# Kernel tuning notes

Hardware: AMD Instinct MI355X
Metric: run time of the kernel (lower is better)

Reference implementation:

```python
import jax, jax.numpy as jnp
import numpy as np

B, C_IN, HW = 4096, 3, 32
NUM_MODULES, NUM_AGENTS, OUT_DIM = 16, 10, 10
FEAT = 128
HID = 48
BN_EPS = 1e-5


def _conv_block(x, w, b):
    # x: [B,C,H,W], w: [O,I,3,3] -> conv(pad=1) + ReLU + maxpool2
    y = jax.lax.conv_general_dilated(
        x, w, window_strides=(1, 1), padding=((1, 1), (1, 1)),
        dimension_numbers=("NCHW", "OIHW", "NCHW"))
    y = jax.nn.relu(y + b[None, :, None, None])
    return jax.lax.reduce_window(y, -jnp.inf, jax.lax.max,
                                 (1, 1, 2, 2), (1, 1, 2, 2), "VALID")


def setup_inputs() -> dict:
    key = jax.random.key(0)
    ks = jax.random.split(key, 24)

    def lin(k, shape, fan_in):
        return (jax.random.normal(k, shape, dtype=jnp.float32) / np.sqrt(fan_in)).astype(jnp.float32)

    inp = {
        "x": jax.random.normal(ks[0], (B, C_IN, HW, HW), dtype=jnp.float32),
        "tasks": jax.random.randint(ks[1], (B,), 0, NUM_AGENTS, dtype=jnp.int32),
        # conv backbone
        "cw1": lin(ks[2], (32, C_IN, 3, 3), C_IN * 9), "cb1": jnp.zeros((32,), jnp.float32),
        "cw2": lin(ks[3], (32, 32, 3, 3), 32 * 9),     "cb2": jnp.zeros((32,), jnp.float32),
        "cw3": lin(ks[4], (32, 32, 3, 3), 32 * 9),     "cb3": jnp.zeros((32,), jnp.float32),
        "cw4": lin(ks[5], (32, 32, 3, 3), 32 * 9),     "cb4": jnp.zeros((32,), jnp.float32),
        "bn_g": jnp.ones((32,), jnp.float32), "bn_b": jnp.zeros((32,), jnp.float32),
        # routing policies (approx linear policies)
        "wpt": lin(ks[6], (FEAT, NUM_AGENTS), FEAT),                  # per-task assignment (1 agent)
        "wd1": lin(ks[7], (NUM_AGENTS, FEAT, NUM_MODULES), FEAT),    # per-agent decision 1
        "wd2": lin(ks[8], (NUM_AGENTS, HID, NUM_MODULES), HID),      # per-agent decision 2
        "wd3": lin(ks[9], (NUM_AGENTS, HID, NUM_MODULES), HID),      # per-agent decision 3
        # expert banks (stacked Linear layers, stored [in,out])
        "s1_w": lin(ks[10], (NUM_MODULES, FEAT, HID), FEAT), "s1_b": jnp.zeros((NUM_MODULES, HID), jnp.float32),
        "s2_w": lin(ks[11], (NUM_MODULES, HID, HID), HID),   "s2_b": jnp.zeros((NUM_MODULES, HID), jnp.float32),
        "s3_w": lin(ks[12], (NUM_MODULES, HID, OUT_DIM), HID), "s3_b": jnp.zeros((NUM_MODULES, OUT_DIM), jnp.float32),
    }
    return inp


def _decide(feat, wd, agents):
    # gather per-sample agent policy, pick argmax action
    logits = jnp.einsum("bf,bfm->bm", feat, wd[agents])  # [B, num_modules]
    return jnp.argmax(logits, axis=-1)


def _select(feat, w_bank, b_bank, actions, relu=True):
    # per-sample expert gather -> small GEMM -> scatter back (vectorized)
    y = jnp.einsum("bf,bfo->bo", feat, w_bank[actions]) + b_bank[actions]
    return jax.nn.relu(y) if relu else y


def reference(x, tasks, cw1, cb1, cw2, cb2, cw3, cb3, cw4, cb4, bn_g, bn_b,
              wpt, wd1, wd2, wd3, s1_w, s1_b, s2_w, s2_b, s3_w, s3_b):
    y = _conv_block(x, cw1, cb1)
    y = _conv_block(y, cw2, cb2)
    y = _conv_block(y, cw3, cb3)
    y = _conv_block(y, cw4, cb4)
    # BatchNorm2d (training-mode batch stats)
    mu = jnp.mean(y, axis=(0, 2, 3), keepdims=True)
    var = jnp.var(y, axis=(0, 2, 3), keepdims=True)
    y = (y - mu) * jax.lax.rsqrt(var + BN_EPS) * bn_g[None, :, None, None] + bn_b[None, :, None, None]
    y = y.reshape(y.shape[0], -1)  # [B, 128]

    # per-task assignment: single-agent policy picks the agent id per sample
    task_actions = jnp.argmax(y @ wpt, axis=-1)  # [B]

    a1 = _decide(y, wd1, task_actions)
    y = _select(y, s1_w, s1_b, a1, relu=True)
    a2 = _decide(y, wd2, task_actions)
    y = _select(y, s2_w, s2_b, a2, relu=True)
    a3 = _decide(y, wd3, task_actions)
    y = _select(y, s3_w, s3_b, a3, relu=False)
    return y
```

## Files before the change

kernel.cpp:

```cpp
#include <hip/hip_runtime.h>
#include <math.h>


#define IMG_B 4096

typedef _Float16 f16x8 __attribute__((ext_vector_type(8)));
typedef _Float16 f16x4 __attribute__((ext_vector_type(4)));
typedef float    f32x4 __attribute__((ext_vector_type(4)));

union U16x8 { unsigned u[4]; f16x8 v; };

__device__ inline f16x8 f16x8_zero() {
    f16x8 z;
    #pragma unroll
    for (int i = 0; i < 8; ++i) z[i] = (_Float16)0.f;
    return z;
}

__global__ __launch_bounds__(256) void twt_kernel(
    const float* __restrict__ cw1, const float* __restrict__ cw2,
    const float* __restrict__ cw3, const float* __restrict__ cw4,
    _Float16* __restrict__ w1s, _Float16* __restrict__ w2s,
    _Float16* __restrict__ w3s, _Float16* __restrict__ w4s)
{
    const int i = blockIdx.x * 256 + threadIdx.x;
    if (i < 2048) {
        const int p = i >> 10, rr = i & 1023;
        const int oc = rr >> 5, k = rr & 31;
        _Float16 val = (_Float16)0.f;
        if (k < 27) {
            float w = cw1[oc * 27 + k];
            _Float16 h = (_Float16)w;
            val = p ? (_Float16)(w - (float)h) : h;
        }
        w1s[p * 1024 + oc * 32 + k] = val;
    }
    if (i < 9216) {
        const int k = i % 9, r = i / 9;
        const int ic2 = r & 31, oc2 = r >> 5;
        {
            float w = cw2[(oc2 * 32 + ic2) * 9 + k];
            _Float16 h = (_Float16)w;
            w2s[(k * 2 + 0) * 1024 + oc2 * 32 + ic2] = h;
            w2s[(k * 2 + 1) * 1024 + oc2 * 32 + ic2] = (_Float16)(w - (float)h);
        }
        {
            float w = cw3[(oc2 * 32 + ic2) * 9 + k];
            _Float16 h = (_Float16)w;
            w3s[(k * 2 + 0) * 1024 + oc2 * 32 + ic2] = h;
            w3s[(k * 2 + 1) * 1024 + oc2 * 32 + ic2] = (_Float16)(w - (float)h);
        }
        {
            float w = cw4[(oc2 * 32 + ic2) * 9 + k];
            _Float16 h = (_Float16)w;
            w4s[(k * 2 + 0) * 1024 + oc2 * 32 + ic2] = h;
            w4s[(k * 2 + 1) * 1024 + oc2 * 32 + ic2] = (_Float16)(w - (float)h);
        }
    }
}

__global__ __launch_bounds__(512, 6) void backbone_kernel(
    const float* __restrict__ x,
    const _Float16* __restrict__ w1s, const float* __restrict__ cb1,
    const _Float16* __restrict__ w2s, const float* __restrict__ cb2,
    const _Float16* __restrict__ w3s, const float* __restrict__ cb3,
    const _Float16* __restrict__ w4s, const float* __restrict__ cb4,
    float* __restrict__ t4)
{
    __shared__ __align__(16) unsigned char smem[50736];
    _Float16* b1h = (_Float16*)smem;
    _Float16* b1l = (_Float16*)(smem + 18432);
    unsigned char* region2 = smem + 36864;
    unsigned* sxu = (unsigned*)region2;
    _Float16* b2h = (_Float16*)region2;
    _Float16* b2l = (_Float16*)(region2 + 4096);
    _Float16* b3h = (_Float16*)(region2 + 8192);
    _Float16* b3l = (_Float16*)(region2 + 10496);
    float*    scr = (float*)region2;

    const int t = threadIdx.x;
    const int b = blockIdx.x;
    const int lane = t & 63;
    const int w  = __builtin_amdgcn_readfirstlane(t >> 6);
    const int wr = w >> 1;
    const int mh = w & 1;
    const int xl = lane & 15;
    const int g  = lane >> 4;
    const int aoff = xl * 32 + g * 8;

    for (int i = t; i < 3468; i += 512) sxu[i] = 0;
    for (int i = t; i < 1024; i += 512) {
        const int j = i & 15, cs = (i >> 4) & 1, r = (i >> 5) & 15, P = i >> 9;
        ((unsigned*)(smem + P * 18432))[(r * 18 + (cs ? 17 : 0)) * 16 + j] = 0;
    }
    __syncthreads();

    {
        const float* xb = x + (size_t)b * 3072;
        for (int i = t; i < 3072; i += 512) {
            const int ic = i >> 10, r = i & 1023;
            const float v = xb[i];
            const _Float16 h = (_Float16)v;
            const _Float16 l = (_Float16)(v - (float)h);
            const unsigned hu = (unsigned)__builtin_bit_cast(unsigned short, h);
            const unsigned lu = (unsigned)__builtin_bit_cast(unsigned short, l);
            sxu[ic * 1156 + ((r >> 5) + 1) * 34 + (r & 31) + 1] = hu | (lu << 16);
        }
    }
    __syncthreads();

    {
        const f16x8 ah0 = *(const f16x8*)(w1s + xl * 32 + g * 8);
        const f16x8 ah1 = *(const f16x8*)(w1s + (16 + xl) * 32 + g * 8);
        const f16x8 al0 = *(const f16x8*)(w1s + 1024 + xl * 32 + g * 8);
        const f16x8 al1 = *(const f16x8*)(w1s + 1024 + (16 + xl) * 32 + g * 8);
        const f32x4 cbias0 = *(const f32x4*)(cb1 + g * 4);
        const f32x4 cbias1 = *(const f32x4*)(cb1 + 16 + g * 4);

        int off_j[8];
        #pragma unroll
        for (int j = 0; j < 8; ++j) {
            int k = g * 8 + j; if (k > 26) k = 26;
            const int ic = k / 9, t9 = k - ic * 9;
            const int dy = t9 / 3, dx = t9 - dy * 3;
            off_j[j] = ic * 1156 + dy * 34 + dx;
        }

        for (int q = 0; q < 2; ++q) {
            const int rp = w * 2 + q;
            const int y0 = 2 * rp;
            for (int xt = 0; xt < 2; ++xt) {
                const int xpix = xt * 16 + xl;
                f32x4 acc[2][2];
                #pragma unroll
                for (int yy = 0; yy < 2; ++yy)
                    #pragma unroll
                    for (int m = 0; m < 2; ++m)
                        #pragma unroll
                        for (int r = 0; r < 4; ++r) acc[yy][m][r] = 0.f;
                #pragma unroll
                for (int yy = 0; yy < 2; ++yy) {
                    const int base = (y0 + yy) * 34 + xpix;
                    unsigned e[8];
                    #pragma unroll
                    for (int j = 0; j < 8; ++j) e[j] = sxu[off_j[j] + base];
                    U16x8 Bh, Bl;
                    #pragma unroll
                    for (int p = 0; p < 4; ++p) {
                        const unsigned e0 = e[2 * p], e1 = e[2 * p + 1];
                        Bh.u[p] = (e0 & 0xffffu) | (e1 << 16);
                        Bl.u[p] = (e0 >> 16) | (e1 & 0xffff0000u);
                    }
                    acc[yy][0] = __builtin_amdgcn_mfma_f32_16x16x32_f16(ah0, Bh.v, acc[yy][0], 0, 0, 0);
                    acc[yy][0] = __builtin_amdgcn_mfma_f32_16x16x32_f16(ah0, Bl.v, acc[yy][0], 0, 0, 0);
                    acc[yy][0] = __builtin_amdgcn_mfma_f32_16x16x32_f16(al0, Bh.v, acc[yy][0], 0, 0, 0);
                    acc[yy][1] = __builtin_amdgcn_mfma_f32_16x16x32_f16(ah1, Bh.v, acc[yy][1], 0, 0, 0);
                    acc[yy][1] = __builtin_amdgcn_mfma_f32_16x16x32_f16(ah1, Bl.v, acc[yy][1], 0, 0, 0);
                    acc[yy][1] = __builtin_amdgcn_mfma_f32_16x16x32_f16(al1, Bh.v, acc[yy][1], 0, 0, 0);
                }
                #pragma unroll
                for (int m = 0; m < 2; ++m) {
                    f32x4 vv;
                    #pragma unroll
                    for (int r = 0; r < 4; ++r) {
                        float v = fmaxf(acc[0][m][r], acc[1][m][r]);
                        v = fmaxf(v, __shfl_xor(v, 1));
                        vv[r] = fmaxf(v + (m ? cbias1[r] : cbias0[r]), 0.f);
                    }
                    if ((xl & 1) == 0) {
                        const int c = xt * 8 + (xl >> 1) + 1;
                        const int grp = m * 2 + (g >> 1);
                        const int so = (grp + (c >> 1)) & 3;
                        const int e = (rp * 18 + c) * 32 + so * 8 + (g & 1) * 4;
                        f16x4 h4, l4;
                        #pragma unroll
                        for (int r = 0; r < 4; ++r) {
                            const _Float16 h = (_Float16)vv[r];
                            h4[r] = h;
                            l4[r] = (_Float16)(vv[r] - (float)h);
                        }
                        *(f16x4*)(b1h + e) = h4;
                        *(f16x4*)(b1l + e) = l4;
                    }
                }
            }
        }
    }
    __syncthreads();

    {
        for (int i = t; i < 1152; i += 512) ((unsigned*)(region2 + 8192))[i] = 0;

        f32x4 acc[2][2];
        #pragma unroll
        for (int j = 0; j < 2; ++j)
            #pragma unroll
            for (int m = 0; m < 2; ++m)
                #pragma unroll
                for (int r = 0; r < 4; ++r) acc[j][m][r] = 0.f;

        #pragma unroll
        for (int dy = 0; dy < 3; ++dy) {
            #pragma unroll
            for (int dx = 0; dx < 3; ++dx) {
                const _Float16* wb = w2s + (dy * 3 + dx) * 2048;
                const f16x8 ah0 = *(const f16x8*)(wb + aoff);
                const f16x8 ah1 = *(const f16x8*)(wb + 512 + aoff);
                const f16x8 al0 = *(const f16x8*)(wb + 1024 + aoff);
                const f16x8 al1 = *(const f16x8*)(wb + 1536 + aoff);

                const int cxs = xl + dx;
                const int so = (g + (cxs >> 1)) & 3;
                #pragma unroll
                for (int j = 0; j < 2; ++j) {
                    const int sy = 2 * w + j + dy - 1;
                    if ((unsigned)sy < 16u) {
                        const int e = (sy * 18 + cxs) * 32 + so * 8;
                        const f16x8 bh = *(const f16x8*)(b1h + e);
                        const f16x8 bl = *(const f16x8*)(b1l + e);
                        acc[j][0] = __builtin_amdgcn_mfma_f32_16x16x32_f16(ah0, bh, acc[j][0], 0, 0, 0);
                        acc[j][0] = __builtin_amdgcn_mfma_f32_16x16x32_f16(ah0, bl, acc[j][0], 0, 0, 0);
                        acc[j][0] = __builtin_amdgcn_mfma_f32_16x16x32_f16(al0, bh, acc[j][0], 0, 0, 0);
                        acc[j][1] = __builtin_amdgcn_mfma_f32_16x16x32_f16(ah1, bh, acc[j][1], 0, 0, 0);
                        acc[j][1] = __builtin_amdgcn_mfma_f32_16x16x32_f16(ah1, bl, acc[j][1], 0, 0, 0);
                        acc[j][1] = __builtin_amdgcn_mfma_f32_16x16x32_f16(al1, bh, acc[j][1], 0, 0, 0);
                    }
                }
            }
        }

        const f32x4 bias0 = *(const f32x4*)(cb2 + g * 4);
        const f32x4 bias1 = *(const f32x4*)(cb2 + 16 + g * 4);
        #pragma unroll
        for (int m = 0; m < 2; ++m) {
            f32x4 vv;
            #pragma unroll
            for (int r = 0; r < 4; ++r) {
                float v = fmaxf(acc[0][m][r], acc[1][m][r]);
                v = fmaxf(v, __shfl_xor(v, 1));
                vv[r] = fmaxf(v + (m ? bias1[r] : bias0[r]), 0.f);
            }
            if ((lane & 1) == 0) {
                const int pp = w * 8 + (xl >> 1);
                const int slot = m * 2 + (g >> 1);
                const int so2 = (slot + (pp >> 1)) & 3;
                const int e = pp * 32 + so2 * 8 + (g & 1) * 4;
                f16x4 h4, l4;
                #pragma unroll
                for (int r = 0; r < 4; ++r) {
                    const _Float16 h = (_Float16)vv[r];
                    h4[r] = h;
                    l4[r] = (_Float16)(vv[r] - (float)h);
                }
                *(f16x4*)(b2h + e) = h4;
                *(f16x4*)(b2l + e) = l4;
            }
        }
    }
    __syncthreads();

    {
        const int p = wr * 16 + xl;
        const int py3 = p >> 3, px3 = p & 7;
        f32x4 acc;
        #pragma unroll
        for (int r = 0; r < 4; ++r) acc[r] = 0.f;

        #pragma unroll
        for (int dy = 0; dy < 3; ++dy) {
            #pragma unroll
            for (int dx = 0; dx < 3; ++dx) {
                const _Float16* wb = w3s + (dy * 3 + dx) * 2048 + mh * 512;
                const f16x8 ah = *(const f16x8*)(wb + aoff);
                const f16x8 al = *(const f16x8*)(wb + 1024 + aoff);

                const int syL = py3 + dy - 1, sxL = px3 + dx - 1;
                const bool ok = ((unsigned)syL < 8u) && ((unsigned)sxL < 8u);
                const int cy = syL < 0 ? 0 : (syL > 7 ? 7 : syL);
                const int cx = sxL < 0 ? 0 : (sxL > 7 ? 7 : sxL);
                const int cp = cy * 8 + cx;
                const int so = (g + (cp >> 1)) & 3;
                const int e = cp * 32 + so * 8;
                f16x8 bh = *(const f16x8*)(b2h + e);
                f16x8 bl = *(const f16x8*)(b2l + e);
                if (!ok) { bh = f16x8_zero(); bl = f16x8_zero(); }
                acc = __builtin_amdgcn_mfma_f32_16x16x32_f16(ah, bh, acc, 0, 0, 0);
                acc = __builtin_amdgcn_mfma_f32_16x16x32_f16(ah, bl, acc, 0, 0, 0);
                acc = __builtin_amdgcn_mfma_f32_16x16x32_f16(al, bh, acc, 0, 0, 0);
            }
        }

        const f32x4 bias = *(const f32x4*)(cb3 + mh * 16 + g * 4);
        f32x4 vv;
        #pragma unroll
        for (int r = 0; r < 4; ++r) {
            float v = acc[r];
            v = fmaxf(v, __shfl_xor(v, 1));
            v = fmaxf(v, __shfl_xor(v, 8));
            vv[r] = fmaxf(v + bias[r], 0.f);
        }
        if ((lane & 9) == 0) {
            const int yr = wr;
            const int xr = (xl & 7) >> 1;
            const int pp3 = (yr + 1) * 6 + (xr + 1);
            const int grp = mh * 2 + (g >> 1);
            const int so = (grp + (pp3 >> 1)) & 3;
            const int e = pp3 * 32 + so * 8 + (g & 1) * 4;
            f16x4 h4, l4;
            #pragma unroll
            for (int r = 0; r < 4; ++r) {
                const _Float16 h = (_Float16)vv[r];
                h4[r] = h;
                l4[r] = (_Float16)(vv[r] - (float)h);
            }
            *(f16x4*)(b3h + e) = h4;
            *(f16x4*)(b3l + e) = l4;
        }
    }
    __syncthreads();

    {
        f32x4 a4;
        #pragma unroll
        for (int r = 0; r < 4; ++r) a4[r] = 0.f;

        for (int t9 = wr; t9 < 9; t9 += 4) {
            const _Float16* wb = w4s + t9 * 2048 + mh * 512;
            const f16x8 ah = *(const f16x8*)(wb + aoff);
            const f16x8 al = *(const f16x8*)(wb + 1024 + aoff);
            const int dy = t9 / 3, dx = t9 - dy * 3;
            const int pp3 = ((xl >> 2) + dy) * 6 + (xl & 3) + dx;
            const int so = (g + (pp3 >> 1)) & 3;
            const int e = pp3 * 32 + so * 8;
            const f16x8 bh = *(const f16x8*)(b3h + e);
            const f16x8 bl = *(const f16x8*)(b3l + e);
            a4 = __builtin_amdgcn_mfma_f32_16x16x32_f16(ah, bh, a4, 0, 0, 0);
            a4 = __builtin_amdgcn_mfma_f32_16x16x32_f16(ah, bl, a4, 0, 0, 0);
            a4 = __builtin_amdgcn_mfma_f32_16x16x32_f16(al, bh, a4, 0, 0, 0);
        }
        *(f32x4*)(scr + (w * 64 + lane) * 4) = a4;
        __syncthreads();

        if (w < 2) {
            f32x4 r0;
            #pragma unroll
            for (int r = 0; r < 4; ++r) r0[r] = 0.f;
            #pragma unroll
            for (int k = 0; k < 4; ++k) {
                const f32x4 p0 = *(const f32x4*)(scr + ((k * 2 + w) * 64 + lane) * 4);
                #pragma unroll
                for (int r = 0; r < 4; ++r) r0[r] += p0[r];
            }
            const f32x4 bias = *(const f32x4*)(cb4 + w * 16 + g * 4);
            const int y = xl >> 2, xx = xl & 3;
            f32x4 vv;
            #pragma unroll
            for (int r = 0; r < 4; ++r) {
                float v = r0[r];
                v = fmaxf(v, __shfl_xor(v, 1));
                v = fmaxf(v, __shfl_xor(v, 4));
                vv[r] = fmaxf(v + bias[r], 0.f);
            }
            if ((xl & 5) == 0) {
                const int oc0 = w * 16 + g * 4;
                #pragma unroll
                for (int r = 0; r < 4; ++r)
                    t4[(size_t)b * 128 + (oc0 + r) * 4 + (y >> 1) * 2 + (xx >> 1)] = vv[r];
            }
        }
    }
}

__global__ __launch_bounds__(256) void bnstats_kernel(
    const float* __restrict__ t4, float* __restrict__ mus, float* __restrict__ rss)
{
    __shared__ double ssum[256];
    __shared__ double ssq[256];
    const int c = blockIdx.x, t = threadIdx.x;
    double s = 0.0, q = 0.0;
    for (int j = t; j < 16384; j += 256) {
        float v = t4[(size_t)(j >> 2) * 128 + c * 4 + (j & 3)];
        s += (double)v;
        q += (double)v * (double)v;
    }
    ssum[t] = s; ssq[t] = q;
    __syncthreads();
    for (int w = 128; w > 0; w >>= 1) {
        if (t < w) { ssum[t] += ssum[t + w]; ssq[t] += ssq[t + w]; }
        __syncthreads();
    }
    if (t == 0) {
        double mu = ssum[0] / 16384.0;
        double var = ssq[0] / 16384.0 - mu * mu;
        mus[c] = (float)mu;
        rss[c] = (float)(1.0 / sqrt(var + 1e-5));
    }
}

__global__ __launch_bounds__(64) void routing_kernel(
    const float* __restrict__ t4, const float* __restrict__ mus,
    const float* __restrict__ rss,
    const float* __restrict__ bng, const float* __restrict__ bnb,
    const float* __restrict__ wpt, const float* __restrict__ wd1,
    const float* __restrict__ wd2, const float* __restrict__ wd3,
    const float* __restrict__ s1w, const float* __restrict__ s1b,
    const float* __restrict__ s2w, const float* __restrict__ s2b,
    const float* __restrict__ s3w, const float* __restrict__ s3b,
    float* __restrict__ out)
{
    __shared__ float f[128];
    __shared__ float h1s[48];
    __shared__ float h2s[48];
    __shared__ float tmp[16];
    __shared__ int act;
    const int t = threadIdx.x, b = blockIdx.x;

    for (int i = t; i < 128; i += 64) {
        int c = i >> 2;
        float v = t4[(size_t)b * 128 + i];
        f[i] = (v - mus[c]) * rss[c] * bng[c] + bnb[c];
    }
    __syncthreads();

    if (t < 10) {
        double a = 0.0;
        for (int k = 0; k < 128; ++k) a = fma((double)f[k], (double)wpt[k * 10 + t], a);
        tmp[t] = (float)a;
    }
    __syncthreads();
    if (t == 0) {
        int bi = 0; float bv = tmp[0];
        for (int i = 1; i < 10; ++i) if (tmp[i] > bv) { bv = tmp[i]; bi = i; }
        act = bi;
    }
    __syncthreads();
    const int agent = act;

    if (t < 16) {
        double a = 0.0;
        const float* wd = wd1 + (size_t)agent * 128 * 16 + t;
        for (int k = 0; k < 128; ++k) a = fma((double)f[k], (double)wd[k * 16], a);
        tmp[t] = (float)a;
    }
    __syncthreads();
    if (t == 0) {
        int bi = 0; float bv = tmp[0];
        for (int i = 1; i < 16; ++i) if (tmp[i] > bv) { bv = tmp[i]; bi = i; }
        act = bi;
    }
    __syncthreads();
    const int a1 = act;

    if (t < 48) {
        float a = s1b[a1 * 48 + t];
        const float* wd = s1w + (size_t)a1 * 128 * 48 + t;
        for (int k = 0; k < 128; ++k) a = fmaf(f[k], wd[k * 48], a);
        h1s[t] = fmaxf(a, 0.f);
    }
    __syncthreads();

    if (t < 16) {
        double a = 0.0;
        const float* wd = wd2 + (size_t)agent * 48 * 16 + t;
        for (int k = 0; k < 48; ++k) a = fma((double)h1s[k], (double)wd[k * 16], a);
        tmp[t] = (float)a;
    }
    __syncthreads();
    if (t == 0) {
        int bi = 0; float bv = tmp[0];
        for (int i = 1; i < 16; ++i) if (tmp[i] > bv) { bv = tmp[i]; bi = i; }
        act = bi;
    }
    __syncthreads();
    const int a2 = act;

    if (t < 48) {
        float a = s2b[a2 * 48 + t];
        const float* wd = s2w + (size_t)a2 * 48 * 48 + t;
        for (int k = 0; k < 48; ++k) a = fmaf(h1s[k], wd[k * 48], a);
        h2s[t] = fmaxf(a, 0.f);
    }
    __syncthreads();

    if (t < 16) {
        double a = 0.0;
        const float* wd = wd3 + (size_t)agent * 48 * 16 + t;
        for (int k = 0; k < 48; ++k) a = fma((double)h2s[k], (double)wd[k * 16], a);
        tmp[t] = (float)a;
    }
    __syncthreads();
    if (t == 0) {
        int bi = 0; float bv = tmp[0];
        for (int i = 1; i < 16; ++i) if (tmp[i] > bv) { bv = tmp[i]; bi = i; }
        act = bi;
    }
    __syncthreads();
    const int a3 = act;

    if (t < 10) {
        float a = s3b[a3 * 10 + t];
        const float* wd = s3w + (size_t)a3 * 48 * 10 + t;
        for (int k = 0; k < 48; ++k) a = fmaf(h2s[k], wd[k * 10], a);
        out[(size_t)b * 10 + t] = a;
    }
}

extern "C" void kernel_launch(void* const* d_in, const int* in_sizes, int n_in,
                              void* d_out, int out_size, void* d_ws, size_t ws_size,
                              hipStream_t stream)
{
    (void)in_sizes; (void)n_in; (void)out_size; (void)ws_size;

    const float* x   = (const float*)d_in[0];
    const float* cw1 = (const float*)d_in[2];
    const float* cb1 = (const float*)d_in[3];
    const float* cw2 = (const float*)d_in[4];
    const float* cb2 = (const float*)d_in[5];
    const float* cw3 = (const float*)d_in[6];
    const float* cb3 = (const float*)d_in[7];
    const float* cw4 = (const float*)d_in[8];
    const float* cb4 = (const float*)d_in[9];
    const float* bng = (const float*)d_in[10];
    const float* bnb = (const float*)d_in[11];
    const float* wpt = (const float*)d_in[12];
    const float* wd1 = (const float*)d_in[13];
    const float* wd2 = (const float*)d_in[14];
    const float* wd3 = (const float*)d_in[15];
    const float* s1w = (const float*)d_in[16];
    const float* s1b = (const float*)d_in[17];
    const float* s2w = (const float*)d_in[18];
    const float* s2b = (const float*)d_in[19];
    const float* s3w = (const float*)d_in[20];
    const float* s3b = (const float*)d_in[21];
    float* out = (float*)d_out;

    float* t4  = (float*)d_ws;
    float* mus = t4 + (size_t)IMG_B * 128;
    float* rss = mus + 32;
    _Float16* w1s = (_Float16*)(rss + 32);
    _Float16* w2s = w1s + 2048;
    _Float16* w3s = w2s + 18432;
    _Float16* w4s = w3s + 18432;

    hipLaunchKernelGGL(twt_kernel, dim3(36), dim3(256), 0, stream,
                       cw1, cw2, cw3, cw4, w1s, w2s, w3s, w4s);
    hipLaunchKernelGGL(backbone_kernel, dim3(IMG_B), dim3(512), 0, stream,
                       x, w1s, cb1, w2s, cb2, w3s, cb3, w4s, cb4, t4);
    hipLaunchKernelGGL(bnstats_kernel, dim3(32), dim3(256), 0, stream, t4, mus, rss);
    hipLaunchKernelGGL(routing_kernel, dim3(IMG_B), dim3(64), 0, stream,
                       t4, mus, rss, bng, bnb, wpt, wd1, wd2, wd3,
                       s1w, s1b, s2w, s2b, s3w, s3b, out);
}
```

Measured before the change: 194.7 us.

## Zero only input halo, use byte-perm packing, and wave-level routing argmax

The backbone kernel now zeros only the halo border of the padded input tile instead of the whole buffer, and drops one block barrier before loading the input. The hi/lo f16 packing uses v_perm instead of shift/mask sequences. The routing kernel packs four samples per 256-thread block, one wave each, and replaces the shared-memory serial argmax and block barriers with shuffle-based wave argmax and wave barriers. Removing the barrier relies on halo zeroing and interior writes touching disjoint addresses. Ties in the argmax now resolve to the lowest index, as before, and the comparison is done in double rather than float.

```diff
diff --git a/kernel.cpp b/kernel.cpp
--- a/kernel.cpp
+++ b/kernel.cpp
@@ -88,13 +88,19 @@
     const int g  = lane >> 4;
     const int aoff = xl * 32 + g * 8;
 
-    for (int i = t; i < 3468; i += 512) sxu[i] = 0;
+    for (int i = t; i < 396; i += 512) {
+        const int p = i / 132, r = i - p * 132;
+        int row, col;
+        if (r < 34)       { row = 0;       col = r; }
+        else if (r < 68)  { row = 33;      col = r - 34; }
+        else if (r < 100) { row = r - 67;  col = 0; }
+        else              { row = r - 99;  col = 33; }
+        sxu[p * 1156 + row * 34 + col] = 0;
+    }
     for (int i = t; i < 1024; i += 512) {
         const int j = i & 15, cs = (i >> 4) & 1, r = (i >> 5) & 15, P = i >> 9;
         ((unsigned*)(smem + P * 18432))[(r * 18 + (cs ? 17 : 0)) * 16 + j] = 0;
     }
-    __syncthreads();
-
     {
         const float* xb = x + (size_t)b * 3072;
         for (int i = t; i < 3072; i += 512) {
@@ -104,7 +110,8 @@
             const _Float16 l = (_Float16)(v - (float)h);
             const unsigned hu = (unsigned)__builtin_bit_cast(unsigned short, h);
             const unsigned lu = (unsigned)__builtin_bit_cast(unsigned short, l);
-            sxu[ic * 1156 + ((r >> 5) + 1) * 34 + (r & 31) + 1] = hu | (lu << 16);
+            sxu[ic * 1156 + ((r >> 5) + 1) * 34 + (r & 31) + 1] =
+                __builtin_amdgcn_perm(lu, hu, 0x05040100u);
         }
     }
     __syncthreads();
@@ -148,8 +155,8 @@
                     #pragma unroll
                     for (int p = 0; p < 4; ++p) {
                         const unsigned e0 = e[2 * p], e1 = e[2 * p + 1];
-                        Bh.u[p] = (e0 & 0xffffu) | (e1 << 16);
-                        Bl.u[p] = (e0 >> 16) | (e1 & 0xffff0000u);
+                        Bh.u[p] = __builtin_amdgcn_perm(e1, e0, 0x05040100u);
+                        Bl.u[p] = __builtin_amdgcn_perm(e1, e0, 0x07060302u);
                     }
                     acc[yy][0] = __builtin_amdgcn_mfma_f32_16x16x32_f16(ah0, Bh.v, acc[yy][0], 0, 0, 0);
                     acc[yy][0] = __builtin_amdgcn_mfma_f32_16x16x32_f16(ah0, Bl.v, acc[yy][0], 0, 0, 0);
@@ -397,7 +404,17 @@
     }
 }
 
-__global__ __launch_bounds__(64) void routing_kernel(
+__device__ __forceinline__ int wave_argmax16(double v, int idx) {
+    #pragma unroll
+    for (int d = 8; d >= 1; d >>= 1) {
+        const double ov = __shfl_xor(v, d);
+        const int oi = __shfl_xor(idx, d);
+        if (ov > v || (ov == v && oi < idx)) { v = ov; idx = oi; }
+    }
+    return __shfl(idx, 0);
+}
+
+__global__ __launch_bounds__(256) void routing_kernel(
     const float* __restrict__ t4, const float* __restrict__ mus,
     const float* __restrict__ rss,
     const float* __restrict__ bng, const float* __restrict__ bnb,
@@ -408,100 +425,75 @@
     const float* __restrict__ s3w, const float* __restrict__ s3b,
     float* __restrict__ out)
 {
-    __shared__ float f[128];
-    __shared__ float h1s[48];
-    __shared__ float h2s[48];
-    __shared__ float tmp[16];
-    __shared__ int act;
-    const int t = threadIdx.x, b = blockIdx.x;
+    __shared__ float fs[4][128];
+    __shared__ float h1s[4][48];
+    __shared__ float h2s[4][48];
+    const int t = threadIdx.x & 63;
+    const int w = threadIdx.x >> 6;
+    const int b = blockIdx.x * 4 + w;
+    float* fw  = fs[w];
+    float* h1w = h1s[w];
+    float* h2w = h2s[w];
 
     for (int i = t; i < 128; i += 64) {
-        int c = i >> 2;
-        float v = t4[(size_t)b * 128 + i];
-        f[i] = (v - mus[c]) * rss[c] * bng[c] + bnb[c];
-    }
-    __syncthreads();
-
+        const int c = i >> 2;
+        const float v = t4[(size_t)b * 128 + i];
+        fw[i] = (v - mus[c]) * rss[c] * bng[c] + bnb[c];
+    }
+    __builtin_amdgcn_wave_barrier();
+
+    double a = -INFINITY;
     if (t < 10) {
-        double a = 0.0;
-        for (int k = 0; k < 128; ++k) a = fma((double)f[k], (double)wpt[k * 10 + t], a);
-        tmp[t] = (float)a;
-    }
-    __syncthreads();
-    if (t == 0) {
-        int bi = 0; float bv = tmp[0];
-        for (int i = 1; i < 10; ++i) if (tmp[i] > bv) { bv = tmp[i]; bi = i; }
-        act = bi;
-    }
-    __syncthreads();
-    const int agent = act;
-
+        a = 0.0;
+        for (int k = 0; k < 128; ++k) a = fma((double)fw[k], (double)wpt[k * 10 + t], a);
+    }
+    const int agent = wave_argmax16(a, t & 15);
+
+    a = -INFINITY;
     if (t < 16) {
-        double a = 0.0;
-        const float* wd = wd1 + (size_t)agent * 128 * 16 + t;
-        for (int k = 0; k < 128; ++k) a = fma((double)f[k], (double)wd[k * 16], a);
-        tmp[t] = (float)a;
-    }
-    __syncthreads();
-    if (t == 0) {
-        int bi = 0; float bv = tmp[0];
-        for (int i = 1; i < 16; ++i) if (tmp[i] > bv) { bv = tmp[i]; bi = i; }
-        act = bi;
-    }
-    __syncthreads();
-    const int a1 = act;
+        a = 0.0;
+        const float* wd = wd1 + (size_t)agent * 2048 + t;
+        for (int k = 0; k < 128; ++k) a = fma((double)fw[k], (double)wd[k * 16], a);
+    }
+    const int a1 = wave_argmax16(a, t & 15);
 
     if (t < 48) {
-        float a = s1b[a1 * 48 + t];
-        const float* wd = s1w + (size_t)a1 * 128 * 48 + t;
-        for (int k = 0; k < 128; ++k) a = fmaf(f[k], wd[k * 48], a);
-        h1s[t] = fmaxf(a, 0.f);
-    }
-    __syncthreads();
-
+        float acc = s1b[a1 * 48 + t];
+        const float* wd = s1w + (size_t)a1 * 6144 + t;
+        for (int k = 0; k < 128; ++k) acc = fmaf(fw[k], wd[k * 48], acc);
+        h1w[t] = fmaxf(acc, 0.f);
+    }
+    __builtin_amdgcn_wave_barrier();
+
+    a = -INFINITY;
     if (t < 16) {
-        double a = 0.0;
-        const float* wd = wd2 + (size_t)agent * 48 * 16 + t;
-        for (int k = 0; k < 48; ++k) a = fma((double)h1s[k], (double)wd[k * 16], a);
-        tmp[t] = (float)a;
-    }
-    __syncthreads();
-    if (t == 0) {
-        int bi = 0; float bv = tmp[0];
-        for (int i = 1; i < 16; ++i) if (tmp[i] > bv) { bv = tmp[i]; bi = i; }
-        act = bi;
-    }
-    __syncthreads();
-    const int a2 = act;
+        a = 0.0;
+        const float* wd = wd2 + (size_t)agent * 768 + t;
+        for (int k = 0; k < 48; ++k) a = fma((double)h1w[k], (double)wd[k * 16], a);
+    }
+    const int a2 = wave_argmax16(a, t & 15);
 
     if (t < 48) {
-        float a = s2b[a2 * 48 + t];
-        const float* wd = s2w + (size_t)a2 * 48 * 48 + t;
-        for (int k = 0; k < 48; ++k) a = fmaf(h1s[k], wd[k * 48], a);
-        h2s[t] = fmaxf(a, 0.f);
-    }
-    __syncthreads();
-
+        float acc = s2b[a2 * 48 + t];
+        const float* wd = s2w + (size_t)a2 * 2304 + t;
+        for (int k = 0; k < 48; ++k) acc = fmaf(h1w[k], wd[k * 48], acc);
+        h2w[t] = fmaxf(acc, 0.f);
+    }
+    __builtin_amdgcn_wave_barrier();
+
+    a = -INFINITY;
     if (t < 16) {
-        double a = 0.0;
-        const float* wd = wd3 + (size_t)agent * 48 * 16 + t;
-        for (int k = 0; k < 48; ++k) a = fma((double)h2s[k], (double)wd[k * 16], a);
-        tmp[t] = (float)a;
-    }
-    __syncthreads();
-    if (t == 0) {
-        int bi = 0; float bv = tmp[0];
-        for (int i = 1; i < 16; ++i) if (tmp[i] > bv) { bv = tmp[i]; bi = i; }
-        act = bi;
-    }
-    __syncthreads();
-    const int a3 = act;
+        a = 0.0;
+        const float* wd = wd3 + (size_t)agent * 768 + t;
+        for (int k = 0; k < 48; ++k) a = fma((double)h2w[k], (double)wd[k * 16], a);
+    }
+    const int a3 = wave_argmax16(a, t & 15);
 
     if (t < 10) {
-        float a = s3b[a3 * 10 + t];
-        const float* wd = s3w + (size_t)a3 * 48 * 10 + t;
-        for (int k = 0; k < 48; ++k) a = fmaf(h2s[k], wd[k * 10], a);
-        out[(size_t)b * 10 + t] = a;
+        float acc = s3b[a3 * 10 + t];
+        const float* wd = s3w + (size_t)a3 * 480 + t;
+        for (int k = 0; k < 48; ++k) acc = fmaf(h2w[k], wd[k * 10], acc);
+        out[(size_t)b * 10 + t] = acc;
     }
 }
 
@@ -547,7 +539,7 @@
     hipLaunchKernelGGL(backbone_kernel, dim3(IMG_B), dim3(512), 0, stream,
                        x, w1s, cb1, w2s, cb2, w3s, cb3, w4s, cb4, t4);
     hipLaunchKernelGGL(bnstats_kernel, dim3(32), dim3(256), 0, stream, t4, mus, rss);
-    hipLaunchKernelGGL(routing_kernel, dim3(IMG_B), dim3(64), 0, stream,
+    hipLaunchKernelGGL(routing_kernel, dim3(IMG_B / 4), dim3(256), 0, stream,
                        t4, mus, rss, bng, bnb, wpt, wd1, wd2, wd3,
                        s1w, s1b, s2w, s2b, s3w, s3b, out);
 }
```

After: 193.9 us. About the same (-0.4%).
